# Kernel optimization log

Measured on AMD Instinct MI355X. Metric: run time of the kernel, lower is better.

## Reference

```python
import jax, jax.numpy as jnp
import numpy as np

B, T, C, H = 2, 2048, 768, 12
HD = C // H  # head dim = 64
EPS = 1e-5


def layer_norm(x, g, b):
    mu = jnp.mean(x, axis=-1, keepdims=True)
    var = jnp.var(x, axis=-1, keepdims=True)
    return (x - mu) * jax.lax.rsqrt(var + EPS) * g + b


def setup_inputs() -> dict:
    key = jax.random.key(0)
    ks = jax.random.split(key, 5)
    s = 0.02
    return {
        "x": jax.random.normal(ks[0], (B, T, C), jnp.float32),
        "ln1_g": jnp.ones((C,), jnp.float32),
        "ln1_b": jnp.zeros((C,), jnp.float32),
        "W_qkv": jax.random.normal(ks[1], (C, 3 * C), jnp.float32) * s,
        "W_attn_proj": jax.random.normal(ks[2], (C, C), jnp.float32) * s,
        "ln2_g": jnp.ones((C,), jnp.float32),
        "ln2_b": jnp.zeros((C,), jnp.float32),
        "W_fc": jax.random.normal(ks[3], (C, 4 * C), jnp.float32) * s,
        "W_mlp_proj": jax.random.normal(ks[4], (4 * C, C), jnp.float32) * s,
    }


def attention(x, W_qkv, W_attn_proj):
    b, t, c = x.shape
    qkv = x @ W_qkv  # [B,T,3C]
    q, k, v = jnp.split(qkv, 3, axis=-1)
    # [B,H,T,HD]
    q = q.reshape(b, t, H, HD).transpose(0, 2, 1, 3)
    k = k.reshape(b, t, H, HD).transpose(0, 2, 1, 3)
    v = v.reshape(b, t, H, HD).transpose(0, 2, 1, 3)
    att = jnp.einsum("bhqd,bhkd->bhqk", q, k) * (1.0 / np.sqrt(HD).astype(np.float32))
    causal = jnp.tril(jnp.ones((t, t), jnp.bool_))
    att = jnp.where(causal, att, jnp.finfo(att.dtype).min)
    att = jax.nn.softmax(att, axis=-1)
    y = jnp.einsum("bhqk,bhkd->bhqd", att, v)
    y = y.transpose(0, 2, 1, 3).reshape(b, t, c)
    return y @ W_attn_proj


def mlp(x, W_fc, W_mlp_proj):
    h = jax.nn.gelu(x @ W_fc, approximate=False)
    return h @ W_mlp_proj


def reference(x, ln1_g, ln1_b, W_qkv, W_attn_proj, ln2_g, ln2_b, W_fc, W_mlp_proj):
    x = x + attention(layer_norm(x, ln1_g, ln1_b), W_qkv, W_attn_proj)
    x = x + mlp(layer_norm(x, ln2_g, ln2_b), W_fc, W_mlp_proj)
    return x
```

## Files before the change

kernel.cpp:

```cpp
#include <hip/hip_runtime.h>
#include <cstdint>
#include <cstddef>

typedef unsigned short u16;
typedef __attribute__((ext_vector_type(4))) float f32x4;
typedef __attribute__((ext_vector_type(8))) short bf16x8;

__device__ __forceinline__ u16 f2bf(float f) {
  unsigned int u = __builtin_bit_cast(unsigned int, f);
  u += 0x7fffu + ((u >> 16) & 1u);
  return (u16)(u >> 16);
}

__device__ __forceinline__ void gl_lds16(const u16* g, u16* lds_base) {
  __builtin_amdgcn_global_load_lds(
      (const __attribute__((address_space(1))) unsigned int*)g,
      (__attribute__((address_space(3))) unsigned int*)lds_base, 16, 0, 0);
}

__global__ __launch_bounds__(256) void transpose_all(const float* __restrict__ s0,
                                                     const float* __restrict__ s1,
                                                     const float* __restrict__ s2,
                                                     const float* __restrict__ s3,
                                                     u16* __restrict__ d0,
                                                     u16* __restrict__ d1,
                                                     u16* __restrict__ d2,
                                                     u16* __restrict__ d3) {
  __shared__ float tile[32][33];
  int idx = blockIdx.x;
  const float* src; u16* dst; int K, N, t;
  if (idx < 1728)      { src = s0; dst = d0; K = 768;  N = 2304; t = idx; }
  else if (idx < 2304) { src = s1; dst = d1; K = 768;  N = 768;  t = idx - 1728; }
  else if (idx < 4608) { src = s2; dst = d2; K = 768;  N = 3072; t = idx - 2304; }
  else                 { src = s3; dst = d3; K = 3072; N = 768;  t = idx - 4608; }
  int nt_n = N >> 5;
  int n0 = (t % nt_n) * 32, k0 = (t / nt_n) * 32;
  int tx = threadIdx.x & 31, ty = threadIdx.x >> 5;
#pragma unroll
  for (int i = 0; i < 4; ++i)
    tile[ty + i * 8][tx] = src[(size_t)(k0 + ty + i * 8) * N + n0 + tx];
  __syncthreads();
#pragma unroll
  for (int i = 0; i < 4; ++i)
    dst[(size_t)(n0 + ty + i * 8) * K + k0 + tx] = f2bf(tile[tx][ty + i * 8]);
}

__global__ __launch_bounds__(256) void transpose_v(const u16* __restrict__ qkvb,
                                                   u16* __restrict__ vt,
                                                   unsigned int* __restrict__ ctr) {
  __shared__ u16 tile[64 * 72];
  if (blockIdx.x == 0 && blockIdx.y == 0 && threadIdx.x == 0) *ctr = 0u;
  int t0 = blockIdx.x * 64;
  int bh = blockIdx.y;
  int b = bh / 12, h = bh % 12;
  int tid = threadIdx.x;
  int c8 = tid & 7, r = tid >> 3;
#pragma unroll
  for (int i = 0; i < 2; ++i) {
    int rr = r + i * 32;
    *(uint4*)&tile[rr * 72 + c8 * 8] =
        *(const uint4*)&qkvb[(size_t)(b * 2048 + t0 + rr) * 2304 + 1536 + h * 64 + c8 * 8];
  }
  __syncthreads();
#pragma unroll
  for (int i = 0; i < 2; ++i) {
    int dr = r + i * 32;
    u16 tmp[8];
#pragma unroll
    for (int j = 0; j < 8; ++j) tmp[j] = tile[(c8 * 8 + j) * 72 + dr];
    *(uint4*)&vt[((size_t)bh * 64 + dr) * 2048 + t0 + c8 * 8] = *(uint4*)tmp;
  }
}

__global__ __launch_bounds__(192) void ln_rows(const float* __restrict__ x,
                                               const float* __restrict__ g,
                                               const float* __restrict__ bb,
                                               u16* __restrict__ out) {
  int row = blockIdx.x;
  int t = threadIdx.x;
  float4 v = *(const float4*)(x + (size_t)row * 768 + t * 4);
  float s = v.x + v.y + v.z + v.w;
  float sq = v.x * v.x + v.y * v.y + v.z * v.z + v.w * v.w;
#pragma unroll
  for (int o = 32; o > 0; o >>= 1) {
    s += __shfl_down(s, o);
    sq += __shfl_down(sq, o);
  }
  __shared__ float ss[3], s2[3];
  int w = t >> 6;
  if ((t & 63) == 0) { ss[w] = s; s2[w] = sq; }
  __syncthreads();
  s = ss[0] + ss[1] + ss[2];
  sq = s2[0] + s2[1] + s2[2];
  float mu = s * (1.f / 768.f);
  float var = sq * (1.f / 768.f) - mu * mu;
  float rs = rsqrtf(var + 1e-5f);
  float4 gv = *(const float4*)(g + t * 4);
  float4 bv = *(const float4*)(bb + t * 4);
  u16 o4[4];
  o4[0] = f2bf((v.x - mu) * rs * gv.x + bv.x);
  o4[1] = f2bf((v.y - mu) * rs * gv.y + bv.y);
  o4[2] = f2bf((v.z - mu) * rs * gv.z + bv.z);
  o4[3] = f2bf((v.w - mu) * rs * gv.w + bv.w);
  *(uint2*)(out + (size_t)row * 768 + t * 4) = *(uint2*)o4;
}

template <int EPI, int TM>
__global__ __launch_bounds__(256, 3) void gemm_bt(const u16* __restrict__ A,
                                                  const u16* __restrict__ BT,
                                                  int M, int N, int K,
                                                  float* __restrict__ outF,
                                                  u16* __restrict__ outB,
                                                  const float* __restrict__ res) {
  constexpr int MT = TM / 64;
  __shared__ __align__(16) u16 Al[2][TM * 64];
  __shared__ __align__(16) u16 Bl[2][64 * 64];
  int tid = threadIdx.x;
  int lane = tid & 63, w = tid >> 6;
  int l16 = lane & 15, quad = lane >> 4;
  int swz = l16 & 7;
  size_t rowA0 = (size_t)blockIdx.y * TM;
  size_t rowB0 = (size_t)blockIdx.x * 64;

  auto stage = [&](int buf, int k0) {
#pragma unroll
    for (int i = 0; i < TM / 32; ++i) {
      int cbase = (i * 4 + w) * 64;
      int chunk = cbase + lane;
      int r = chunk >> 3, c8 = (chunk & 7) ^ (r & 7);
      gl_lds16(&A[(rowA0 + r) * (size_t)K + k0 + c8 * 8], &Al[buf][cbase * 8]);
    }
#pragma unroll
    for (int i = 0; i < 2; ++i) {
      int cbase = (i * 4 + w) * 64;
      int chunk = cbase + lane;
      int r = chunk >> 3, c8 = (chunk & 7) ^ (r & 7);
      gl_lds16(&BT[(rowB0 + r) * (size_t)K + k0 + c8 * 8], &Bl[buf][cbase * 8]);
    }
  };

  f32x4 acc[MT][4] = {};
  stage(0, 0);
  int cur = 0;
  for (int k0 = 0; k0 < K; k0 += 64) {
    __syncthreads();
    if (k0 + 64 < K) stage(cur ^ 1, k0 + 64);
#pragma unroll
    for (int ks = 0; ks < 2; ++ks) {
      int c = ks * 4 + quad;
      bf16x8 af[MT], bf[4];
#pragma unroll
      for (int mt = 0; mt < MT; ++mt)
        af[mt] = *(const bf16x8*)&Al[cur][(w * (TM / 4) + mt * 16 + l16) * 64 + (c ^ swz) * 8];
#pragma unroll
      for (int nt = 0; nt < 4; ++nt)
        bf[nt] = *(const bf16x8*)&Bl[cur][(nt * 16 + l16) * 64 + (c ^ swz) * 8];
#pragma unroll
      for (int mt = 0; mt < MT; ++mt)
#pragma unroll
        for (int nt = 0; nt < 4; ++nt)
          acc[mt][nt] = __builtin_amdgcn_mfma_f32_16x16x32_bf16(af[mt], bf[nt], acc[mt][nt], 0, 0, 0);
    }
    cur ^= 1;
  }

#pragma unroll
  for (int mt = 0; mt < MT; ++mt) {
#pragma unroll
    for (int i = 0; i < 4; ++i) {
      size_t row = rowA0 + w * (TM / 4) + mt * 16 + quad * 4 + i;
#pragma unroll
      for (int nt = 0; nt < 4; ++nt) {
        size_t col = rowB0 + nt * 16 + l16;
        float v = acc[mt][nt][i];
        if (EPI == 0) {
          outB[row * N + col] = f2bf(v);
        } else if (EPI == 1) {
          outF[row * N + col] = res[row * N + col] + v;
        } else {
          float ge = 0.5f * v * (1.f + erff(v * 0.70710678118654752f));
          outB[row * N + col] = f2bf(ge);
        }
      }
    }
  }
}

__global__ __launch_bounds__(256, 3) void flash_attn(const u16* __restrict__ qkv,
                                                     const u16* __restrict__ vt,
                                                     u16* __restrict__ y,
                                                     unsigned int* __restrict__ ctr) {
  __shared__ __align__(16) u16 Kl[128 * 64];
  __shared__ __align__(16) u16 Vl[64 * 128];
  __shared__ __align__(16) u16 Pl[4][16 * 136];
  __shared__ unsigned int s_unit;

  int tid = threadIdx.x;
  int lane = tid & 63, w = tid >> 6;
  int l16 = lane & 15, quad = lane >> 4;
  int swz = l16 & 7;
  u16* Pw = &Pl[w][0];

  for (;;) {
    __syncthreads();
    if (tid == 0) s_unit = atomicAdd(ctr, 1u);
    __syncthreads();
    unsigned int u = s_unit;
    if (u >= 768u) return;

    int qt = 31 - (int)(u / 24u);
    int bh = (int)(u % 24u);
    int b = bh / 12, h = bh % 12;
    int qw = qt * 64 + w * 16;

    const u16* base = qkv + (size_t)b * 2048 * 2304;
    const u16* vbase = vt + (size_t)bh * 64 * 2048;

    bf16x8 qf0, qf1;
    {
      const u16* qp = base + (size_t)(qw + l16) * 2304 + h * 64 + quad * 8;
      qf0 = *(const bf16x8*)qp;
      qf1 = *(const bf16x8*)(qp + 32);
    }

    f32x4 O[4] = {};
    float l_i[4] = {0.f, 0.f, 0.f, 0.f};

    int nkb = qt / 2 + 1;
    const float sc = 0.125f * 1.44269504088896340736f;
    for (int kb = 0; kb < nkb; ++kb) {
      int kt0 = kb << 7;
      __syncthreads();
#pragma unroll
      for (int i = 0; i < 4; ++i) {
        int cbase = (i * 4 + w) * 64;
        int chunk = cbase + lane;
        int r = chunk >> 3, c8 = (chunk & 7) ^ (r & 7);
        gl_lds16(base + (size_t)(kt0 + r) * 2304 + 768 + h * 64 + c8 * 8, &Kl[cbase * 8]);
      }
#pragma unroll
      for (int i = 0; i < 4; ++i) {
        int cbase = (i * 4 + w) * 64;
        int chunk = cbase + lane;
        int r = chunk >> 4, c16 = (chunk & 15) ^ (r & 7);
        gl_lds16(vbase + (size_t)r * 2048 + kt0 + c16 * 8, &Vl[cbase * 8]);
      }
      __syncthreads();

      f32x4 S[8];
#pragma unroll
      for (int nt = 0; nt < 8; ++nt) {
        bf16x8 k0 = *(const bf16x8*)&Kl[(nt * 16 + l16) * 64 + (quad ^ swz) * 8];
        bf16x8 k1 = *(const bf16x8*)&Kl[(nt * 16 + l16) * 64 + ((4 + quad) ^ swz) * 8];
        f32x4 z = {};
        z = __builtin_amdgcn_mfma_f32_16x16x32_bf16(qf0, k0, z, 0, 0, 0);
        S[nt] = __builtin_amdgcn_mfma_f32_16x16x32_bf16(qf1, k1, z, 0, 0, 0);
      }

      bool diag = (kb == nkb - 1);
#pragma unroll
      for (int nt = 0; nt < 8; ++nt) {
        int tk = kt0 + nt * 16 + l16;
#pragma unroll
        for (int i = 0; i < 4; ++i) {
          float p = exp2f(S[nt][i] * sc);
          if (diag && tk > qw + quad * 4 + i) p = 0.f;
          l_i[i] += p;
          Pw[(quad * 4 + i) * 136 + nt * 16 + l16] =
              (u16)(__builtin_bit_cast(unsigned int, p) >> 16);
        }
      }

      asm volatile("s_waitcnt lgkmcnt(0)" ::: "memory");

#pragma unroll
      for (int c = 0; c < 4; ++c) {
        bf16x8 pf = *(const bf16x8*)&Pw[l16 * 136 + c * 32 + quad * 8];
#pragma unroll
        for (int dt = 0; dt < 4; ++dt) {
          bf16x8 vf = *(const bf16x8*)&Vl[(dt * 16 + l16) * 128 + ((c * 4 + quad) ^ swz) * 8];
          O[dt] = __builtin_amdgcn_mfma_f32_16x16x32_bf16(pf, vf, O[dt], 0, 0, 0);
        }
      }
    }

#pragma unroll
    for (int i = 0; i < 4; ++i) {
#pragma unroll
      for (int o = 1; o < 16; o <<= 1) l_i[i] += __shfl_xor(l_i[i], o);
    }
#pragma unroll
    for (int dt = 0; dt < 4; ++dt) {
#pragma unroll
      for (int i = 0; i < 4; ++i) {
        int tq = qw + quad * 4 + i;
        float ov = O[dt][i] / l_i[i];
        y[(size_t)(b * 2048 + tq) * 768 + h * 64 + dt * 16 + l16] = f2bf(ov);
      }
    }
  }
}

extern "C" void kernel_launch(void* const* d_in, const int* in_sizes, int n_in,
                              void* d_out, int out_size, void* d_ws, size_t ws_size,
                              hipStream_t stream) {
  const float* x      = (const float*)d_in[0];
  const float* ln1_g  = (const float*)d_in[1];
  const float* ln1_b  = (const float*)d_in[2];
  const float* W_qkv  = (const float*)d_in[3];
  const float* W_attn = (const float*)d_in[4];
  const float* ln2_g  = (const float*)d_in[5];
  const float* ln2_b  = (const float*)d_in[6];
  const float* W_fc   = (const float*)d_in[7];
  const float* W_mlp  = (const float*)d_in[8];
  float* out = (float*)d_out;

  const int M = 4096;
  char* p = (char*)d_ws;
  auto alloc = [&](size_t bytes) {
    char* r = p;
    p += (bytes + 255) & ~(size_t)255;
    return r;
  };
  u16* wt_qkv  = (u16*)alloc((size_t)2304 * 768 * 2);
  u16* wt_attn = (u16*)alloc((size_t)768 * 768 * 2);
  u16* wt_fc   = (u16*)alloc((size_t)3072 * 768 * 2);
  u16* wt_mlp  = (u16*)alloc((size_t)768 * 3072 * 2);
  u16* xn1     = (u16*)alloc((size_t)M * 768 * 2);
  u16* qkvb    = (u16*)alloc((size_t)M * 2304 * 2);
  u16* yb      = (u16*)alloc((size_t)M * 768 * 2);
  float* x1    = (float*)alloc((size_t)M * 768 * 4);
  u16* xn2     = (u16*)alloc((size_t)M * 768 * 2);
  u16* hb      = (u16*)alloc((size_t)M * 3072 * 2);
  u16* vt      = (u16*)alloc((size_t)24 * 64 * 2048 * 2);
  unsigned int* ctr = (unsigned int*)alloc(256);

  transpose_all<<<6912, 256, 0, stream>>>(W_qkv, W_attn, W_fc, W_mlp,
                                          wt_qkv, wt_attn, wt_fc, wt_mlp);

  ln_rows<<<M, 192, 0, stream>>>(x, ln1_g, ln1_b, xn1);
  gemm_bt<0, 128><<<dim3(2304 / 64, M / 128), 256, 0, stream>>>(xn1, wt_qkv, M, 2304, 768,
                                                                nullptr, qkvb, nullptr);
  transpose_v<<<dim3(32, 24), 256, 0, stream>>>(qkvb, vt, ctr);
  flash_attn<<<768, 256, 0, stream>>>(qkvb, vt, yb, ctr);
  gemm_bt<1, 64><<<dim3(768 / 64, M / 64), 256, 0, stream>>>(yb, wt_attn, M, 768, 768,
                                                             x1, nullptr, x);
  ln_rows<<<M, 192, 0, stream>>>(x1, ln2_g, ln2_b, xn2);
  gemm_bt<2, 128><<<dim3(3072 / 64, M / 128), 256, 0, stream>>>(xn2, wt_fc, M, 3072, 768,
                                                                nullptr, hb, nullptr);
  gemm_bt<1, 64><<<dim3(768 / 64, M / 64), 256, 0, stream>>>(hb, wt_mlp, M, 768, 3072,
                                                             out, nullptr, x1);
}
```

Measured before the change: 271.8 us.

## Split heavy causal attention tiles across two work units and prefetch K

Query tiles in the upper half of the sequence are split along the key dimension into two work units that write unnormalized partial outputs and row sums to scratch. A new combine kernel sums the partials and normalizes them. The goal is to balance load across workgroups and shorten the tail caused by long causal rows. The K tile for the next block is now staged into LDS while the current block's PV product runs, with an extra barrier per iteration. The cost is an extra kernel launch, fp32 partial traffic, and reuse of the MLP hidden buffer as scratch.

```diff
diff --git a/kernel.cpp b/kernel.cpp
--- a/kernel.cpp
+++ b/kernel.cpp
@@ -189,6 +189,8 @@
 __global__ __launch_bounds__(256, 3) void flash_attn(const u16* __restrict__ qkv,
                                                      const u16* __restrict__ vt,
                                                      u16* __restrict__ y,
+                                                     float* __restrict__ OP,
+                                                     float* __restrict__ LP,
                                                      unsigned int* __restrict__ ctr) {
   __shared__ __align__(16) u16 Kl[128 * 64];
   __shared__ __align__(16) u16 Vl[64 * 128];
@@ -206,12 +208,26 @@
     if (tid == 0) s_unit = atomicAdd(ctr, 1u);
     __syncthreads();
     unsigned int u = s_unit;
-    if (u >= 768u) return;
-
-    int qt = 31 - (int)(u / 24u);
-    int bh = (int)(u % 24u);
+    if (u >= 1152u) return;
+
+    int qt, bh, kb0, kb1, part;
+    bool heavy;
+    if (u < 384u) {
+      int t = (int)u;
+      qt = 31 - t / 24; bh = t % 24;
+      part = 0; kb0 = 0; kb1 = 8; heavy = true;
+    } else if (u < 768u) {
+      int t = (int)u - 384;
+      qt = 31 - t / 24; bh = t % 24;
+      part = 1; kb0 = 8; kb1 = qt / 2 + 1; heavy = true;
+    } else {
+      int t = (int)u - 768;
+      qt = 15 - t / 24; bh = t % 24;
+      part = 0; kb0 = 0; kb1 = qt / 2 + 1; heavy = false;
+    }
     int b = bh / 12, h = bh % 12;
     int qw = qt * 64 + w * 16;
+    int kdiag = qt / 2;
 
     const u16* base = qkv + (size_t)b * 2048 * 2304;
     const u16* vbase = vt + (size_t)bh * 64 * 2048;
@@ -226,11 +242,9 @@
     f32x4 O[4] = {};
     float l_i[4] = {0.f, 0.f, 0.f, 0.f};
 
-    int nkb = qt / 2 + 1;
     const float sc = 0.125f * 1.44269504088896340736f;
-    for (int kb = 0; kb < nkb; ++kb) {
-      int kt0 = kb << 7;
-      __syncthreads();
+
+    auto stageK = [&](int kt0) {
 #pragma unroll
       for (int i = 0; i < 4; ++i) {
         int cbase = (i * 4 + w) * 64;
@@ -238,6 +252,8 @@
         int r = chunk >> 3, c8 = (chunk & 7) ^ (r & 7);
         gl_lds16(base + (size_t)(kt0 + r) * 2304 + 768 + h * 64 + c8 * 8, &Kl[cbase * 8]);
       }
+    };
+    auto stageV = [&](int kt0) {
 #pragma unroll
       for (int i = 0; i < 4; ++i) {
         int cbase = (i * 4 + w) * 64;
@@ -245,7 +261,13 @@
         int r = chunk >> 4, c16 = (chunk & 15) ^ (r & 7);
         gl_lds16(vbase + (size_t)r * 2048 + kt0 + c16 * 8, &Vl[cbase * 8]);
       }
+    };
+
+    stageK(kb0 << 7);
+    for (int kb = kb0; kb < kb1; ++kb) {
+      int kt0 = kb << 7;
       __syncthreads();
+      stageV(kt0);
 
       f32x4 S[8];
 #pragma unroll
@@ -257,7 +279,7 @@
         S[nt] = __builtin_amdgcn_mfma_f32_16x16x32_bf16(qf1, k1, z, 0, 0, 0);
       }
 
-      bool diag = (kb == nkb - 1);
+      bool diag = (kb == kdiag);
 #pragma unroll
       for (int nt = 0; nt < 8; ++nt) {
         int tk = kt0 + nt * 16 + l16;
@@ -271,7 +293,8 @@
         }
       }
 
-      asm volatile("s_waitcnt lgkmcnt(0)" ::: "memory");
+      __syncthreads();
+      if (kb + 1 < kb1) stageK((kb + 1) << 7);
 
 #pragma unroll
       for (int c = 0; c < 4; ++c) {
@@ -289,16 +312,54 @@
 #pragma unroll
       for (int o = 1; o < 16; o <<= 1) l_i[i] += __shfl_xor(l_i[i], o);
     }
-#pragma unroll
-    for (int dt = 0; dt < 4; ++dt) {
-#pragma unroll
-      for (int i = 0; i < 4; ++i) {
-        int tq = qw + quad * 4 + i;
-        float ov = O[dt][i] / l_i[i];
-        y[(size_t)(b * 2048 + tq) * 768 + h * 64 + dt * 16 + l16] = f2bf(ov);
-      }
-    }
-  }
+
+    if (heavy) {
+      size_t tno = (size_t)(bh * 16 + (qt - 16)) * 2 + part;
+      float* op = OP + tno * 4096;
+      float* lp = LP + tno * 64;
+#pragma unroll
+      for (int dt = 0; dt < 4; ++dt) {
+#pragma unroll
+        for (int i = 0; i < 4; ++i)
+          op[(w * 16 + quad * 4 + i) * 64 + dt * 16 + l16] = O[dt][i];
+      }
+      if (l16 == 0) {
+#pragma unroll
+        for (int i = 0; i < 4; ++i) lp[w * 16 + quad * 4 + i] = l_i[i];
+      }
+    } else {
+#pragma unroll
+      for (int dt = 0; dt < 4; ++dt) {
+#pragma unroll
+        for (int i = 0; i < 4; ++i) {
+          int tq = qw + quad * 4 + i;
+          float ov = O[dt][i] / l_i[i];
+          y[(size_t)(b * 2048 + tq) * 768 + h * 64 + dt * 16 + l16] = f2bf(ov);
+        }
+      }
+    }
+  }
+}
+
+__global__ __launch_bounds__(256) void attn_combine(const float* __restrict__ OP,
+                                                    const float* __restrict__ LP,
+                                                    u16* __restrict__ y) {
+  int t = blockIdx.x;
+  int bh = t >> 4, qth = t & 15;
+  int b = bh / 12, h = bh % 12;
+  int tid = threadIdx.x;
+  int r = tid >> 2;
+  int c0 = (tid & 3) << 4;
+  const float* a = OP + (size_t)t * 2 * 4096 + r * 64 + c0;
+  const float* bp = a + 4096;
+  float inv = 1.f / (LP[(size_t)t * 128 + r] + LP[(size_t)t * 128 + 64 + r]);
+  u16 ob[16];
+#pragma unroll
+  for (int j = 0; j < 16; ++j) ob[j] = f2bf((a[j] + bp[j]) * inv);
+  size_t row = (size_t)b * 2048 + (size_t)(16 + qth) * 64 + r;
+  u16* yp = y + row * 768 + h * 64 + c0;
+  *(uint4*)yp = *(uint4*)&ob[0];
+  *(uint4*)(yp + 8) = *(uint4*)&ob[8];
 }
 
 extern "C" void kernel_launch(void* const* d_in, const int* in_sizes, int n_in,
@@ -335,6 +396,9 @@
   u16* vt      = (u16*)alloc((size_t)24 * 64 * 2048 * 2);
   unsigned int* ctr = (unsigned int*)alloc(256);
 
+  float* OPb = (float*)hb;
+  float* LPb = OPb + (size_t)24 * 16 * 2 * 4096;
+
   transpose_all<<<6912, 256, 0, stream>>>(W_qkv, W_attn, W_fc, W_mlp,
                                           wt_qkv, wt_attn, wt_fc, wt_mlp);
 
@@ -342,7 +406,8 @@
   gemm_bt<0, 128><<<dim3(2304 / 64, M / 128), 256, 0, stream>>>(xn1, wt_qkv, M, 2304, 768,
                                                                 nullptr, qkvb, nullptr);
   transpose_v<<<dim3(32, 24), 256, 0, stream>>>(qkvb, vt, ctr);
-  flash_attn<<<768, 256, 0, stream>>>(qkvb, vt, yb, ctr);
+  flash_attn<<<768, 256, 0, stream>>>(qkvb, vt, yb, OPb, LPb, ctr);
+  attn_combine<<<384, 256, 0, stream>>>(OPb, LPb, yb);
   gemm_bt<1, 64><<<dim3(768 / 64, M / 64), 256, 0, stream>>>(yb, wt_attn, M, 768, 768,
                                                              x1, nullptr, x);
   ln_rows<<<M, 192, 0, stream>>>(x1, ln2_g, ln2_b, xn2);
```

New measurement: 271.7 us. No clear change (-0.0%).
